# Optimization experiments

Hardware: AMD Instinct MI355X
Metric: run time of the kernel (lower is better)

The kernel has to match this reference:

```python
import jax, jax.numpy as jnp
import numpy as np
from math import sqrt

N = 8192      # points
I = 16        # in_channels
H = 64        # hidden_units
O = 64        # out_channels
CUTS = 8      # conv MLP intermediate width
RADIUS = 9.0
GROUPS = 4    # GroupNorm groups
BLK = 128     # i-block size for tiled pairwise reduction (KeOps-style)


def _leaky(x):
    return jnp.where(x >= 0, x, 0.2 * x)


def _group_norm(f, w, b, eps=1e-5):
    # torch GroupNorm applied to (1, C, N): stats per group over (C//G channels x N points)
    n, c = f.shape
    g = f.reshape(n, GROUPS, c // GROUPS)
    m = g.mean(axis=(0, 2), keepdims=True)
    v = ((g - m) ** 2).mean(axis=(0, 2), keepdims=True)
    g = (g - m) * jax.lax.rsqrt(v + eps)
    return g.reshape(n, c) * w + b


def setup_inputs() -> dict:
    key = jax.random.key(0)
    ks = jax.random.split(key, 20)
    U = lambda k, s, lim: jax.random.uniform(k, s, minval=-lim, maxval=lim)
    points = jax.random.normal(ks[0], (N, 3), dtype=jnp.float32)
    nuv = jax.random.normal(ks[1], (N, 3, 3), dtype=jnp.float32)
    features = jax.random.normal(ks[2], (N, I), dtype=jnp.float32)
    # net_in (torch Linear default init)
    W_in1 = U(ks[3], (H, I), 1 / np.sqrt(I)); b_in1 = U(ks[4], (H,), 1 / np.sqrt(I))
    W_in2 = U(ks[5], (H, H), 1 / np.sqrt(H)); b_in2 = U(ks[6], (H,), 1 / np.sqrt(H))
    # conv MLP with custom init from the module
    A1 = jax.random.normal(ks[7], (CUTS, 3), dtype=jnp.float32)
    B1 = jax.random.uniform(ks[8], (CUTS,)) * 0.8 * jnp.sqrt((A1 ** 2).sum(-1))
    A2 = U(ks[9], (H, CUTS), 1 / np.sqrt(CUTS))
    B2 = jax.random.normal(ks[10], (H,)) * 0.5 * jnp.sqrt((A2 ** 2).sum(-1))
    # net_out
    W_out1 = U(ks[11], (O, H), 1 / np.sqrt(H)); b_out1 = U(ks[12], (O,), 1 / np.sqrt(H))
    W_out2 = U(ks[13], (O, O), 1 / np.sqrt(O)); b_out2 = U(ks[14], (O,), 1 / np.sqrt(O))
    return {
        "points": points, "nuv": nuv, "features": features,
        "W_in1": W_in1, "b_in1": b_in1, "W_in2": W_in2, "b_in2": b_in2,
        "gn_in_w": jnp.ones((H,), jnp.float32), "gn_in_b": jnp.zeros((H,), jnp.float32),
        "A1": A1, "B1": B1, "A2": A2, "B2": B2,
        "W_out1": W_out1, "b_out1": b_out1, "W_out2": W_out2, "b_out2": b_out2,
        "gn_out_w": jnp.ones((O,), jnp.float32), "gn_out_b": jnp.zeros((O,), jnp.float32),
    }


def _forward(points, nuv, features, W_in1, b_in1, W_in2, b_in2, gn_in_w, gn_in_b,
             A1, B1, A2, B2, W_out1, b_out1, W_out2, b_out2, gn_out_w, gn_out_b):
    # 1. net_in + GroupNorm
    f = _leaky(features @ W_in1.T + b_in1)
    f = _leaky(f @ W_in2.T + b_in2)
    f = _group_norm(f, gn_in_w, gn_in_b)          # (N, H)
    # 2. quasi-geodesic interaction, tiled over i-blocks (KeOps-style)
    pts = points / (sqrt(2.0) * RADIUS)
    normals = jax.lax.stop_gradient(nuv[:, 0, :])  # n_j is detached in the original
    nblk = N // BLK

    def body(carry, blk):
        xi, nuvi = blk                              # (B,3), (B,3,3)
        ni = nuvi[:, 0, :]                          # (B,3) n_i (not detached)
        diff = pts[None, :, :] - xi[:, None, :]     # (B,N,3) x_j - x_i
        dn = ni @ normals.T                         # (B,N) <n_i, n_j>
        d2 = (diff ** 2).sum(-1) * (2.0 - dn) ** 2  # pseudo-geodesic squared dist
        w = jnp.exp(-d2)                            # Gaussian window
        X = jnp.einsum('bij,bnj->bni', nuvi, diff)  # coords in local basis (B,N,3)
        h = jax.nn.relu(jnp.einsum('bnj,cj->bnc', X, A1) + B1)   # (B,N,CUTS)
        g = jax.nn.relu(jnp.einsum('bnc,hc->bnh', h, A2) + B2)   # (B,N,H)
        out = jnp.einsum('bn,bnh,nh->bh', w, g, f)  # sum_j w_ij * conv(P_ij) * f_j
        return carry, out

    _, outs = jax.lax.scan(
        body, None, (pts.reshape(nblk, BLK, 3), nuv.reshape(nblk, BLK, 3, 3)))
    f2 = outs.reshape(N, H)
    # 3. net_out + GroupNorm
    f2 = _leaky(f2 @ W_out1.T + b_out1)
    f2 = _leaky(f2 @ W_out2.T + b_out2)
    f2 = _group_norm(f2, gn_out_w, gn_out_b)       # (N, O)
    return f2


def reference(points, nuv, features, W_in1, b_in1, W_in2, b_in2, gn_in_w, gn_in_b,
              A1, B1, A2, B2, W_out1, b_out1, W_out2, b_out2, gn_out_w, gn_out_b):
    return _forward(points, nuv, features, W_in1, b_in1, W_in2, b_in2, gn_in_w, gn_in_b,
                    A1, B1, A2, B2, W_out1, b_out1, W_out2, b_out2, gn_out_w, gn_out_b)
```

## Files before the change

### kernel.cpp

```cpp
#include <hip/hip_runtime.h>
#include <hip/hip_bf16.h>
#include <stdint.h>


#define N_PTS   8192
#define CHUNK   64
#define NCHUNK  (N_PTS / CHUNK)
#define WPB     8
#define PSCALE  0.07856742013183861f
#define GN_CNT  (N_PTS * 16)
#define FS_STRIDE 68

#define OFF_POINTS 0
#define OFF_NUV    24576
#define OFF_FEAT   98304
#define OFF_WIN1   229376
#define OFF_BIN1   230400
#define OFF_WIN2   230464
#define OFF_BIN2   234560
#define OFF_GNIW   234624
#define OFF_GNIB   234688
#define OFF_A1     234752
#define OFF_B1     234776
#define OFF_A2     234784
#define OFF_B2     235296
#define OFF_WOUT1  235360
#define OFF_BOUT1  239456
#define OFF_WOUT2  239520
#define OFF_BOUT2  243616
#define OFF_GNOW   243680
#define OFF_GNOB   243744
#define CVT_TOTAL  243808
#define NSEG 19

typedef _Float16 half2_t __attribute__((ext_vector_type(2)));
typedef _Float16 f16x8   __attribute__((ext_vector_type(8)));
typedef float    f32x4   __attribute__((ext_vector_type(4)));

struct InPtrs { const void* p[NSEG]; };

__device__ __forceinline__ float rfl(float x) {
  return __int_as_float(__builtin_amdgcn_readfirstlane(__float_as_int(x)));
}
__device__ __forceinline__ float leaky(float x) { return x > 0.f ? x : 0.2f * x; }

#if __has_builtin(__builtin_amdgcn_cvt_pkrtz)
__device__ __forceinline__ half2_t pk16(float a, float b) {
  return __builtin_bit_cast(half2_t, __builtin_amdgcn_cvt_pkrtz(a, b));
}
#else
__device__ __forceinline__ half2_t pk16(float a, float b) {
  half2_t r; r.x = (_Float16)a; r.y = (_Float16)b; return r;
}
#endif

__global__ __launch_bounds__(256) void prep_kernel(InPtrs ptrs, float* dst,
                                                   float* gstats) {
  if (blockIdx.x == 0 && threadIdx.x < 16) gstats[threadIdx.x] = 0.f;
  const uint32_t w0 = ((const uint32_t*)ptrs.p[7])[0];
  const bool bf = (w0 != 0x3F800000u);
  const int CUM[NSEG + 1] = {0, 24576, 98304, 229376, 230400, 230464, 234560,
                             234624, 234688, 234752, 234776, 234784, 235296,
                             235360, 239456, 239520, 243616, 243680, 243744,
                             243808};
  for (int e = blockIdx.x * 256 + threadIdx.x; e < CVT_TOTAL;
       e += gridDim.x * 256) {
    int s = 0;
#pragma unroll
    for (int i = 1; i < NSEG; ++i) s += (e >= CUM[i]) ? 1 : 0;
    const int rem = e - CUM[s];
    float v = bf ? __bfloat162float(((const __hip_bfloat16*)ptrs.p[s])[rem])
                 : ((const float*)ptrs.p[s])[rem];
    if (s == 0) v *= PSCALE;
    dst[e] = v;
  }
}

__global__ __launch_bounds__(256) void mlp_in_kernel(
    const float* __restrict__ pool, float* __restrict__ fbuf) {
  __shared__ float ls[4][64];
  const int t = threadIdx.x, nl = t >> 6, h = t & 63;
  const int n = blockIdx.x * 4 + nl;
  const float4* fr = (const float4*)(pool + OFF_FEAT + n * 16);
  const float4* w1 = (const float4*)(pool + OFF_WIN1 + h * 16);
  float a = pool[OFF_BIN1 + h];
#pragma unroll
  for (int k = 0; k < 4; ++k) {
    const float4 x = fr[k], w = w1[k];
    a = fmaf(x.x, w.x, a); a = fmaf(x.y, w.y, a);
    a = fmaf(x.z, w.z, a); a = fmaf(x.w, w.w, a);
  }
  ls[nl][h] = leaky(a);
  __syncthreads();
  const float4* w2 = (const float4*)(pool + OFF_WIN2 + h * 64);
  const float4* lr = (const float4*)&ls[nl][0];
  float c = pool[OFF_BIN2 + h];
#pragma unroll
  for (int k = 0; k < 16; ++k) {
    const float4 x = lr[k], w = w2[k];
    c = fmaf(x.x, w.x, c); c = fmaf(x.y, w.y, c);
    c = fmaf(x.z, w.z, c); c = fmaf(x.w, w.w, c);
  }
  fbuf[n * 64 + h] = leaky(c);
}

__global__ __launch_bounds__(256) void mlp_out_kernel(
    const float* __restrict__ cbuf, const float* __restrict__ pool,
    float* __restrict__ obuf) {
  __shared__ float ls[4][64];
  const int t = threadIdx.x, nl = t >> 6, h = t & 63;
  const int n = blockIdx.x * 4 + nl;
  const float4* cr = (const float4*)(cbuf + n * 64);
  const float4* w1 = (const float4*)(pool + OFF_WOUT1 + h * 64);
  float a = pool[OFF_BOUT1 + h];
#pragma unroll
  for (int k = 0; k < 16; ++k) {
    const float4 x = cr[k], w = w1[k];
    a = fmaf(x.x, w.x, a); a = fmaf(x.y, w.y, a);
    a = fmaf(x.z, w.z, a); a = fmaf(x.w, w.w, a);
  }
  ls[nl][h] = leaky(a);
  __syncthreads();
  const float4* w2 = (const float4*)(pool + OFF_WOUT2 + h * 64);
  const float4* lr = (const float4*)&ls[nl][0];
  float c = pool[OFF_BOUT2 + h];
#pragma unroll
  for (int k = 0; k < 16; ++k) {
    const float4 x = lr[k], w = w2[k];
    c = fmaf(x.x, w.x, c); c = fmaf(x.y, w.y, c);
    c = fmaf(x.z, w.z, c); c = fmaf(x.w, w.w, c);
  }
  obuf[n * 64 + h] = leaky(c);
}

__global__ __launch_bounds__(256) void gn_stats_kernel(
    const float* __restrict__ buf, float* __restrict__ gstats) {
  __shared__ float red[8];
  const int t = threadIdx.x;
  const int g = (t & 63) >> 4;
  if (t < 8) red[t] = 0.f;
  float s = 0.f, q = 0.f;
  for (int idx = blockIdx.x * 256 + t; idx < N_PTS * 64; idx += 64 * 256) {
    const float v = buf[idx];
    s += v; q = fmaf(v, v, q);
  }
  __syncthreads();
  atomicAdd(&red[g], s);
  atomicAdd(&red[4 + g], q);
  __syncthreads();
  if (t < 8) atomicAdd(&gstats[t], red[t]);
}

__global__ __launch_bounds__(256) void gn_apply_kernel(
    float* __restrict__ buf, const float* __restrict__ gstats,
    const float* __restrict__ pool) {
  const int idx = blockIdx.x * 256 + threadIdx.x;
  const int h = idx & 63, g = h >> 4;
  const float m = gstats[g] * (1.f / GN_CNT);
  const float v = gstats[4 + g] * (1.f / GN_CNT) - m * m;
  const float rs = rsqrtf(fmaxf(v, 0.f) + 1e-5f);
  buf[idx] = fmaf((buf[idx] - m) * rs, pool[OFF_GNIW + h], pool[OFF_GNIB + h]);
}

__global__ __launch_bounds__(256) void gn_apply_out_kernel(
    const float* __restrict__ buf, const float* __restrict__ gstats,
    const float* __restrict__ pool, void* __restrict__ out,
    const uint32_t* __restrict__ dref) {
  const bool bf = (dref[0] != 0x3F800000u);
  const int idx = blockIdx.x * 256 + threadIdx.x;
  const int h = idx & 63, g = h >> 4;
  const float m = gstats[g] * (1.f / GN_CNT);
  const float v = gstats[4 + g] * (1.f / GN_CNT) - m * m;
  const float rs = rsqrtf(fmaxf(v, 0.f) + 1e-5f);
  const float r = fmaf((buf[idx] - m) * rs, pool[OFF_GNOW + h], pool[OFF_GNOB + h]);
  if (bf) ((__hip_bfloat16*)out)[idx] = __float2bfloat16(r);
  else    ((float*)out)[idx] = r;
}

__global__ __launch_bounds__(512) void conv_kernel(
    const float* __restrict__ pool, const float* __restrict__ fbuf,
    float* __restrict__ cbuf) {
  __shared__ float  f_s[CHUNK * FS_STRIDE];
  __shared__ float4 hcA[WPB][4][32];
  __shared__ float4 zero4_s;

  const int t = threadIdx.x;
  const int wv = t >> 6, lane = t & 63;
  const int b = blockIdx.x * WPB + wv;
  const int kg  = lane >> 4;
  const int l15 = lane & 15;

  const float pbx = rfl(pool[OFF_POINTS + b * 3 + 0]);
  const float pby = rfl(pool[OFF_POINTS + b * 3 + 1]);
  const float pbz = rfl(pool[OFF_POINTS + b * 3 + 2]);
  float nb[9];
#pragma unroll
  for (int i = 0; i < 9; ++i) nb[i] = rfl(pool[OFF_NUV + b * 9 + i]);
  float a1v[24], b1v[8];
#pragma unroll
  for (int i = 0; i < 24; ++i) a1v[i] = rfl(pool[OFF_A1 + i]);
#pragma unroll
  for (int i = 0; i < 8; ++i)  b1v[i] = rfl(pool[OFF_B1 + i]);

  f16x8 bfrag[4];
#pragma unroll
  for (int ht = 0; ht < 4; ++ht) {
    const int h = 16 * ht + l15;
#pragma unroll
    for (int i = 0; i < 8; ++i) {
      float v = 0.f;
      if (kg == 0) v = pool[OFF_A2 + h * 8 + i];
      else if (kg == 1 && i == 0) v = pool[OFF_B2 + h];
      bfrag[ht][i] = (_Float16)v;
    }
  }

  {
    float4 z4; z4.x = 0.f; z4.y = 0.f; z4.z = 0.f; z4.w = 0.f;
    if (lane < 32) {
#pragma unroll
      for (int jt = 0; jt < 4; ++jt) hcA[wv][jt][lane] = z4;
    }
    if (t == 0) zero4_s = z4;
  }

  const f32x4 kzero = {0.f, 0.f, 0.f, 0.f};
  float acc[4] = {0.f, 0.f, 0.f, 0.f};
  const float4* fg4 = (const float4*)fbuf;

  for (int c = 0; c < NCHUNK; ++c) {
    const float4 fv0 = fg4[c * 1024 + t];
    const float4 fv1 = fg4[c * 1024 + t + 512];
    const int n = c * CHUNK + lane;
    const float px = pool[OFF_POINTS + n * 3 + 0];
    const float py = pool[OFF_POINTS + n * 3 + 1];
    const float pz = pool[OFF_POINTS + n * 3 + 2];
    const float nx = pool[OFF_NUV + n * 9 + 0];
    const float ny = pool[OFF_NUV + n * 9 + 1];
    const float nz = pool[OFF_NUV + n * 9 + 2];

    __syncthreads();
    ((float4*)f_s)[(t >> 4) * 17 + (t & 15)]        = fv0;
    ((float4*)f_s)[((t >> 4) + 32) * 17 + (t & 15)] = fv1;

    const float dx = px - pbx, dy = py - pby, dz = pz - pbz;
    const float X0 = fmaf(nb[0], dx, fmaf(nb[1], dy, nb[2] * dz));
    const float X1 = fmaf(nb[3], dx, fmaf(nb[4], dy, nb[5] * dz));
    const float X2 = fmaf(nb[6], dx, fmaf(nb[7], dy, nb[8] * dz));
    const float dn = fmaf(nb[0], nx, fmaf(nb[1], ny, nb[2] * nz));
    const float dd = fmaf(dx, dx, fmaf(dy, dy, dz * dz));
    const float tt = 2.f - dn;
    const float w = __expf(-dd * tt * tt);

    float hc[8];
#pragma unroll
    for (int cc = 0; cc < 8; ++cc)
      hc[cc] = w * fmaxf(fmaf(X0, a1v[cc * 3 + 0],
                         fmaf(X1, a1v[cc * 3 + 1],
                         fmaf(X2, a1v[cc * 3 + 2], b1v[cc]))), 0.f);
    float4 lo;
    lo.x = __builtin_bit_cast(float, pk16(hc[0], hc[1]));
    lo.y = __builtin_bit_cast(float, pk16(hc[2], hc[3]));
    lo.z = __builtin_bit_cast(float, pk16(hc[4], hc[5]));
    lo.w = __builtin_bit_cast(float, pk16(hc[6], hc[7]));
    hcA[wv][lane >> 4][l15] = lo;
    ((float*)&hcA[wv][lane >> 4][16 + l15])[0] =
        __builtin_bit_cast(float, pk16(w, 0.f));

    __syncthreads();

#pragma unroll
    for (int jt = 0; jt < 4; ++jt) {
      const float4* ap = (kg < 2) ? &hcA[wv][jt][kg * 16 + l15] : &zero4_s;
      const f16x8 af = __builtin_bit_cast(f16x8, *ap);
      const int fbase = (16 * jt + kg * 4) * FS_STRIDE + l15;
#pragma unroll
      for (int ht = 0; ht < 4; ++ht) {
        const f32x4 D = __builtin_amdgcn_mfma_f32_16x16x32_f16(
            af, bfrag[ht], kzero, 0, 0, 0);
        const float* fb = &f_s[fbase + 16 * ht];
#pragma unroll
        for (int r = 0; r < 4; ++r)
          acc[ht] = fmaf(fb[r * FS_STRIDE], fmaxf(D[r], 0.f), acc[ht]);
      }
    }
  }

#pragma unroll
  for (int ht = 0; ht < 4; ++ht) {
    acc[ht] += __shfl_xor(acc[ht], 16, 64);
    acc[ht] += __shfl_xor(acc[ht], 32, 64);
  }
  if (lane < 16) {
#pragma unroll
    for (int ht = 0; ht < 4; ++ht)
      cbuf[b * 64 + 16 * ht + lane] = acc[ht];
  }
}

extern "C" void kernel_launch(void* const* d_in, const int* in_sizes, int n_in,
                              void* d_out, int out_size, void* d_ws, size_t ws_size,
                              hipStream_t stream) {
  (void)in_sizes; (void)n_in; (void)out_size; (void)ws_size;
  const uint32_t* dref = (const uint32_t*)d_in[7];

  float* pool   = (float*)d_ws;
  float* fbuf   = pool + CVT_TOTAL;
  float* cbuf   = fbuf + N_PTS * 64;
  float* gstats = cbuf + N_PTS * 64;

  InPtrs ptrs;
  for (int i = 0; i < NSEG; ++i) ptrs.p[i] = d_in[i];

  prep_kernel<<<256, 256, 0, stream>>>(ptrs, pool, gstats);
  mlp_in_kernel<<<N_PTS / 4, 256, 0, stream>>>(pool, fbuf);
  gn_stats_kernel<<<64, 256, 0, stream>>>(fbuf, gstats);
  gn_apply_kernel<<<N_PTS * 64 / 256, 256, 0, stream>>>(fbuf, gstats, pool);
  conv_kernel<<<N_PTS / WPB, 512, 0, stream>>>(pool, fbuf, cbuf);
  mlp_out_kernel<<<N_PTS / 4, 256, 0, stream>>>(cbuf, pool, fbuf);
  gn_stats_kernel<<<64, 256, 0, stream>>>(fbuf, gstats + 8);
  gn_apply_out_kernel<<<N_PTS * 64 / 256, 256, 0, stream>>>(
      fbuf, gstats + 8, pool, d_out, dref);
}
```

Before: 695.9 us.

## Fold local-frame transform into A1, prefetch chunk data, use smaller MFMA

The conv kernel now precomputes per-row matrices M = A1·nuv_i and offsets, so each pair needs only one 3x3 affine step instead of a frame projection followed by the A1 layer. Squared distance is computed from packed points with precomputed norms, which a new pack kernel writes. The next chunk's features, points and normals are software-prefetched across the barriers, the K=32 f16 MFMA is replaced by a K=16 variant that wastes fewer zero lanes, and the accumulation uses packed FMA with an occupancy hint added to launch bounds. The risks are cancellation in the |p|^2-2p·q expansion and more register pressure from the prefetch.

```diff
diff --git a/kernel.cpp b/kernel.cpp
--- a/kernel.cpp
+++ b/kernel.cpp
@@ -34,7 +34,8 @@
 #define NSEG 19
 
 typedef _Float16 half2_t __attribute__((ext_vector_type(2)));
-typedef _Float16 f16x8   __attribute__((ext_vector_type(8)));
+typedef _Float16 f16x4   __attribute__((ext_vector_type(4)));
+typedef float    f32x2   __attribute__((ext_vector_type(2)));
 typedef float    f32x4   __attribute__((ext_vector_type(4)));
 
 struct InPtrs { const void* p[NSEG]; };
@@ -74,6 +75,24 @@
     if (s == 0) v *= PSCALE;
     dst[e] = v;
   }
+}
+
+__global__ __launch_bounds__(256) void pack_kernel(
+    const float* __restrict__ pool, float4* __restrict__ ppk,
+    float4* __restrict__ npk) {
+  const int n = blockIdx.x * 256 + threadIdx.x;
+  const float px = pool[OFF_POINTS + n * 3 + 0];
+  const float py = pool[OFF_POINTS + n * 3 + 1];
+  const float pz = pool[OFF_POINTS + n * 3 + 2];
+  float4 p; p.x = px; p.y = py; p.z = pz;
+  p.w = fmaf(px, px, fmaf(py, py, pz * pz));
+  ppk[n] = p;
+  float4 q;
+  q.x = pool[OFF_NUV + n * 9 + 0];
+  q.y = pool[OFF_NUV + n * 9 + 1];
+  q.z = pool[OFF_NUV + n * 9 + 2];
+  q.w = 0.f;
+  npk[n] = q;
 }
 
 __global__ __launch_bounds__(256) void mlp_in_kernel(
@@ -177,12 +196,14 @@
   else    ((float*)out)[idx] = r;
 }
 
-__global__ __launch_bounds__(512) void conv_kernel(
+__global__ __launch_bounds__(512, 8) void conv_kernel(
     const float* __restrict__ pool, const float* __restrict__ fbuf,
-    float* __restrict__ cbuf) {
+    float* __restrict__ cbuf, const float4* __restrict__ ppk,
+    const float4* __restrict__ npk) {
   __shared__ float  f_s[CHUNK * FS_STRIDE];
-  __shared__ float4 hcA[WPB][4][32];
-  __shared__ float4 zero4_s;
+  __shared__ float4 hcA2[WPB][CHUNK];
+  __shared__ f32x2  hcW2[WPB][CHUNK];
+  __shared__ f32x2  zero2_s;
 
   const int t = threadIdx.x;
   const int wv = t >> 6, lane = t & 63;
@@ -196,105 +217,131 @@
   float nb[9];
 #pragma unroll
   for (int i = 0; i < 9; ++i) nb[i] = rfl(pool[OFF_NUV + b * 9 + i]);
-  float a1v[24], b1v[8];
-#pragma unroll
-  for (int i = 0; i < 24; ++i) a1v[i] = rfl(pool[OFF_A1 + i]);
-#pragma unroll
-  for (int i = 0; i < 8; ++i)  b1v[i] = rfl(pool[OFF_B1 + i]);
-
-  f16x8 bfrag[4];
+  const float pbsq = rfl(fmaf(pbx, pbx, fmaf(pby, pby, pbz * pbz)));
+
+  float mM[24], mc[8];
+#pragma unroll
+  for (int cc = 0; cc < 8; ++cc) {
+    const float a0 = pool[OFF_A1 + cc * 3 + 0];
+    const float a1 = pool[OFF_A1 + cc * 3 + 1];
+    const float a2 = pool[OFF_A1 + cc * 3 + 2];
+#pragma unroll
+    for (int j = 0; j < 3; ++j)
+      mM[cc * 3 + j] =
+          rfl(fmaf(a0, nb[j], fmaf(a1, nb[3 + j], a2 * nb[6 + j])));
+    mc[cc] = rfl(fmaf(-mM[cc * 3 + 0], pbx,
+                 fmaf(-mM[cc * 3 + 1], pby,
+                 fmaf(-mM[cc * 3 + 2], pbz, pool[OFF_B1 + cc]))));
+  }
+
+  f16x4 bfrag[4];
 #pragma unroll
   for (int ht = 0; ht < 4; ++ht) {
     const int h = 16 * ht + l15;
 #pragma unroll
-    for (int i = 0; i < 8; ++i) {
+    for (int i = 0; i < 4; ++i) {
+      const int k = 4 * kg + i;
       float v = 0.f;
-      if (kg == 0) v = pool[OFF_A2 + h * 8 + i];
-      else if (kg == 1 && i == 0) v = pool[OFF_B2 + h];
+      if (k < 8) v = pool[OFF_A2 + h * 8 + k];
+      else if (k == 8) v = pool[OFF_B2 + h];
       bfrag[ht][i] = (_Float16)v;
     }
   }
 
-  {
-    float4 z4; z4.x = 0.f; z4.y = 0.f; z4.z = 0.f; z4.w = 0.f;
-    if (lane < 32) {
-#pragma unroll
-      for (int jt = 0; jt < 4; ++jt) hcA[wv][jt][lane] = z4;
-    }
-    if (t == 0) zero4_s = z4;
-  }
-
+  if (t == 0) { zero2_s.x = 0.f; zero2_s.y = 0.f; }
+
+  f32x2 acc01[4], acc23[4];
+#pragma unroll
+  for (int ht = 0; ht < 4; ++ht) {
+    acc01[ht].x = 0.f; acc01[ht].y = 0.f;
+    acc23[ht].x = 0.f; acc23[ht].y = 0.f;
+  }
   const f32x4 kzero = {0.f, 0.f, 0.f, 0.f};
-  float acc[4] = {0.f, 0.f, 0.f, 0.f};
   const float4* fg4 = (const float4*)fbuf;
 
+  float4 fv0 = fg4[t];
+  float4 fv1 = fg4[t + 512];
+  float4 pv  = ppk[lane];
+  float4 nv  = npk[lane];
+
   for (int c = 0; c < NCHUNK; ++c) {
-    const float4 fv0 = fg4[c * 1024 + t];
-    const float4 fv1 = fg4[c * 1024 + t + 512];
-    const int n = c * CHUNK + lane;
-    const float px = pool[OFF_POINTS + n * 3 + 0];
-    const float py = pool[OFF_POINTS + n * 3 + 1];
-    const float pz = pool[OFF_POINTS + n * 3 + 2];
-    const float nx = pool[OFF_NUV + n * 9 + 0];
-    const float ny = pool[OFF_NUV + n * 9 + 1];
-    const float nz = pool[OFF_NUV + n * 9 + 2];
-
-    __syncthreads();
+    asm volatile("" ::: "memory");
+    __builtin_amdgcn_s_barrier();
+    asm volatile("" ::: "memory");
+
     ((float4*)f_s)[(t >> 4) * 17 + (t & 15)]        = fv0;
     ((float4*)f_s)[((t >> 4) + 32) * 17 + (t & 15)] = fv1;
 
-    const float dx = px - pbx, dy = py - pby, dz = pz - pbz;
-    const float X0 = fmaf(nb[0], dx, fmaf(nb[1], dy, nb[2] * dz));
-    const float X1 = fmaf(nb[3], dx, fmaf(nb[4], dy, nb[5] * dz));
-    const float X2 = fmaf(nb[6], dx, fmaf(nb[7], dy, nb[8] * dz));
-    const float dn = fmaf(nb[0], nx, fmaf(nb[1], ny, nb[2] * nz));
-    const float dd = fmaf(dx, dx, fmaf(dy, dy, dz * dz));
-    const float tt = 2.f - dn;
-    const float w = __expf(-dd * tt * tt);
-
+    const float dotp = fmaf(pv.x, pbx, fmaf(pv.y, pby, pv.z * pbz));
+    const float dd   = fmaf(-2.f, dotp, pv.w + pbsq);
+    const float dn   = fmaf(nb[0], nv.x, fmaf(nb[1], nv.y, nb[2] * nv.z));
+    const float ttv  = 2.f - dn;
+    const float wexp = __expf(-dd * ttv * ttv);
     float hc[8];
 #pragma unroll
     for (int cc = 0; cc < 8; ++cc)
-      hc[cc] = w * fmaxf(fmaf(X0, a1v[cc * 3 + 0],
-                         fmaf(X1, a1v[cc * 3 + 1],
-                         fmaf(X2, a1v[cc * 3 + 2], b1v[cc]))), 0.f);
-    float4 lo;
-    lo.x = __builtin_bit_cast(float, pk16(hc[0], hc[1]));
-    lo.y = __builtin_bit_cast(float, pk16(hc[2], hc[3]));
-    lo.z = __builtin_bit_cast(float, pk16(hc[4], hc[5]));
-    lo.w = __builtin_bit_cast(float, pk16(hc[6], hc[7]));
-    hcA[wv][lane >> 4][l15] = lo;
-    ((float*)&hcA[wv][lane >> 4][16 + l15])[0] =
-        __builtin_bit_cast(float, pk16(w, 0.f));
-
-    __syncthreads();
+      hc[cc] = wexp * fmaxf(fmaf(mM[cc * 3 + 0], pv.x,
+                            fmaf(mM[cc * 3 + 1], pv.y,
+                            fmaf(mM[cc * 3 + 2], pv.z, mc[cc]))), 0.f);
+    float4 av;
+    av.x = __builtin_bit_cast(float, pk16(hc[0], hc[1]));
+    av.y = __builtin_bit_cast(float, pk16(hc[2], hc[3]));
+    av.z = __builtin_bit_cast(float, pk16(hc[4], hc[5]));
+    av.w = __builtin_bit_cast(float, pk16(hc[6], hc[7]));
+    hcA2[wv][lane] = av;
+    f32x2 wv2;
+    wv2.x = __builtin_bit_cast(float, pk16(wexp, 0.f));
+    wv2.y = 0.f;
+    hcW2[wv][lane] = wv2;
+
+    const int cn = (c < NCHUNK - 1) ? c + 1 : c;
+    fv0 = fg4[cn * 1024 + t];
+    fv1 = fg4[cn * 1024 + t + 512];
+    pv  = ppk[cn * CHUNK + lane];
+    nv  = npk[cn * CHUNK + lane];
+
+    asm volatile("s_waitcnt lgkmcnt(0)" ::: "memory");
+    __builtin_amdgcn_s_barrier();
+    asm volatile("" ::: "memory");
 
 #pragma unroll
     for (int jt = 0; jt < 4; ++jt) {
-      const float4* ap = (kg < 2) ? &hcA[wv][jt][kg * 16 + l15] : &zero4_s;
-      const f16x8 af = __builtin_bit_cast(f16x8, *ap);
+      const f32x2* ap;
+      if (kg < 2)       ap = ((const f32x2*)&hcA2[wv][16 * jt + l15]) + kg;
+      else if (kg == 2) ap = &hcW2[wv][16 * jt + l15];
+      else              ap = &zero2_s;
+      const f16x4 af = __builtin_bit_cast(f16x4, *ap);
       const int fbase = (16 * jt + kg * 4) * FS_STRIDE + l15;
 #pragma unroll
       for (int ht = 0; ht < 4; ++ht) {
-        const f32x4 D = __builtin_amdgcn_mfma_f32_16x16x32_f16(
+        const f32x4 D = __builtin_amdgcn_mfma_f32_16x16x16f16(
             af, bfrag[ht], kzero, 0, 0, 0);
         const float* fb = &f_s[fbase + 16 * ht];
-#pragma unroll
-        for (int r = 0; r < 4; ++r)
-          acc[ht] = fmaf(fb[r * FS_STRIDE], fmaxf(D[r], 0.f), acc[ht]);
+        f32x2 fq01, fq23, q01, q23;
+        fq01.x = fb[0];             fq01.y = fb[FS_STRIDE];
+        fq23.x = fb[2 * FS_STRIDE]; fq23.y = fb[3 * FS_STRIDE];
+        q01.x = fmaxf(D[0], 0.f);   q01.y = fmaxf(D[1], 0.f);
+        q23.x = fmaxf(D[2], 0.f);   q23.y = fmaxf(D[3], 0.f);
+        asm("v_pk_fma_f32 %0, %1, %2, %0"
+            : "+v"(acc01[ht]) : "v"(fq01), "v"(q01));
+        asm("v_pk_fma_f32 %0, %1, %2, %0"
+            : "+v"(acc23[ht]) : "v"(fq23), "v"(q23));
       }
     }
   }
 
+  float accf[4];
 #pragma unroll
   for (int ht = 0; ht < 4; ++ht) {
-    acc[ht] += __shfl_xor(acc[ht], 16, 64);
-    acc[ht] += __shfl_xor(acc[ht], 32, 64);
+    float a = (acc01[ht].x + acc01[ht].y) + (acc23[ht].x + acc23[ht].y);
+    a += __shfl_xor(a, 16, 64);
+    a += __shfl_xor(a, 32, 64);
+    accf[ht] = a;
   }
   if (lane < 16) {
 #pragma unroll
     for (int ht = 0; ht < 4; ++ht)
-      cbuf[b * 64 + 16 * ht + lane] = acc[ht];
+      cbuf[b * 64 + 16 * ht + lane] = accf[ht];
   }
 }
 
@@ -308,15 +355,20 @@
   float* fbuf   = pool + CVT_TOTAL;
   float* cbuf   = fbuf + N_PTS * 64;
   float* gstats = cbuf + N_PTS * 64;
+  float* ppk    = gstats + 16;
+  float* npk    = ppk + N_PTS * 4;
 
   InPtrs ptrs;
   for (int i = 0; i < NSEG; ++i) ptrs.p[i] = d_in[i];
 
   prep_kernel<<<256, 256, 0, stream>>>(ptrs, pool, gstats);
+  pack_kernel<<<N_PTS / 256, 256, 0, stream>>>(pool, (float4*)ppk, (float4*)npk);
   mlp_in_kernel<<<N_PTS / 4, 256, 0, stream>>>(pool, fbuf);
   gn_stats_kernel<<<64, 256, 0, stream>>>(fbuf, gstats);
   gn_apply_kernel<<<N_PTS * 64 / 256, 256, 0, stream>>>(fbuf, gstats, pool);
-  conv_kernel<<<N_PTS / WPB, 512, 0, stream>>>(pool, fbuf, cbuf);
+  conv_kernel<<<N_PTS / WPB, 512, 0, stream>>>(pool, fbuf, cbuf,
+                                               (const float4*)ppk,
+                                               (const float4*)npk);
   mlp_out_kernel<<<N_PTS / 4, 256, 0, stream>>>(cbuf, pool, fbuf);
   gn_stats_kernel<<<64, 256, 0, stream>>>(fbuf, gstats + 8);
   gn_apply_out_kernel<<<N_PTS * 64 / 256, 256, 0, stream>>>(
```

Result: slower. 805.1 us (+15.7%).

## Transpose normalized features so conv kernel reads them with float4 LDS loads

Applied to the files above, without the earlier changes.

The GroupNorm apply kernel now writes the normalized features transposed (channel-major) into a new buffer through a shared-memory tile. The conv kernel stages these transposed chunks into LDS, so each MFMA output group can fetch its four feature values with a single float4 read instead of four strided scalar reads. This targets LDS instruction count in the hot inner loop. The cost is an extra transpose pass and a second feature buffer in the workspace, which assumes the workspace is large enough.

```diff
diff --git a/kernel.cpp b/kernel.cpp
--- a/kernel.cpp
+++ b/kernel.cpp
@@ -151,15 +151,43 @@
   if (t < 8) atomicAdd(&gstats[t], red[t]);
 }
 
-__global__ __launch_bounds__(256) void gn_apply_kernel(
-    float* __restrict__ buf, const float* __restrict__ gstats,
-    const float* __restrict__ pool) {
-  const int idx = blockIdx.x * 256 + threadIdx.x;
-  const int h = idx & 63, g = h >> 4;
+__global__ __launch_bounds__(256) void gn_apply_T_kernel(
+    const float* __restrict__ buf, const float* __restrict__ gstats,
+    const float* __restrict__ pool, float* __restrict__ bufT) {
+  __shared__ float tile[64][68];
+  const int t = threadIdx.x;
+  const int n0 = blockIdx.x * 64;
+  const int rr = t >> 4;
+  const int cc = (t & 15) * 4;
+  const int g = cc >> 4;
   const float m = gstats[g] * (1.f / GN_CNT);
   const float v = gstats[4 + g] * (1.f / GN_CNT) - m * m;
   const float rs = rsqrtf(fmaxf(v, 0.f) + 1e-5f);
-  buf[idx] = fmaf((buf[idx] - m) * rs, pool[OFF_GNIW + h], pool[OFF_GNIB + h]);
+  const float4 gw = *(const float4*)&pool[OFF_GNIW + cc];
+  const float4 gb = *(const float4*)&pool[OFF_GNIB + cc];
+#pragma unroll
+  for (int r = 0; r < 4; ++r) {
+    const int row = rr + 16 * r;
+    const float4 x = *(const float4*)&buf[(n0 + row) * 64 + cc];
+    float4 o;
+    o.x = fmaf((x.x - m) * rs, gw.x, gb.x);
+    o.y = fmaf((x.y - m) * rs, gw.y, gb.y);
+    o.z = fmaf((x.z - m) * rs, gw.z, gb.z);
+    o.w = fmaf((x.w - m) * rs, gw.w, gb.w);
+    *(float4*)&tile[row][cc] = o;
+  }
+  __syncthreads();
+  const int nb = (t & 15) * 4;
+#pragma unroll
+  for (int r = 0; r < 4; ++r) {
+    const int h = rr + 16 * r;
+    float4 o;
+    o.x = tile[nb + 0][h];
+    o.y = tile[nb + 1][h];
+    o.z = tile[nb + 2][h];
+    o.w = tile[nb + 3][h];
+    *(float4*)&bufT[h * N_PTS + n0 + nb] = o;
+  }
 }
 
 __global__ __launch_bounds__(256) void gn_apply_out_kernel(
@@ -178,9 +206,9 @@
 }
 
 __global__ __launch_bounds__(512) void conv_kernel(
-    const float* __restrict__ pool, const float* __restrict__ fbuf,
+    const float* __restrict__ pool, const float* __restrict__ fbufT,
     float* __restrict__ cbuf) {
-  __shared__ float  f_s[CHUNK * FS_STRIDE];
+  __shared__ float  f_t[CHUNK * FS_STRIDE];
   __shared__ float4 hcA[WPB][4][32];
   __shared__ float4 zero4_s;
 
@@ -226,11 +254,13 @@
 
   const f32x4 kzero = {0.f, 0.f, 0.f, 0.f};
   float acc[4] = {0.f, 0.f, 0.f, 0.f};
-  const float4* fg4 = (const float4*)fbuf;
+  const float4* ftg = (const float4*)fbufT;
+  const int srow = t >> 3;
+  const int scol = (t & 7) * 2;
 
   for (int c = 0; c < NCHUNK; ++c) {
-    const float4 fv0 = fg4[c * 1024 + t];
-    const float4 fv1 = fg4[c * 1024 + t + 512];
+    const float4 fv0 = ftg[srow * (N_PTS / 4) + c * 16 + scol];
+    const float4 fv1 = ftg[srow * (N_PTS / 4) + c * 16 + scol + 1];
     const int n = c * CHUNK + lane;
     const float px = pool[OFF_POINTS + n * 3 + 0];
     const float py = pool[OFF_POINTS + n * 3 + 1];
@@ -240,8 +270,8 @@
     const float nz = pool[OFF_NUV + n * 9 + 2];
 
     __syncthreads();
-    ((float4*)f_s)[(t >> 4) * 17 + (t & 15)]        = fv0;
-    ((float4*)f_s)[((t >> 4) + 32) * 17 + (t & 15)] = fv1;
+    ((float4*)f_t)[srow * 17 + scol]     = fv0;
+    ((float4*)f_t)[srow * 17 + scol + 1] = fv1;
 
     const float dx = px - pbx, dy = py - pby, dz = pz - pbz;
     const float X0 = fmaf(nb[0], dx, fmaf(nb[1], dy, nb[2] * dz));
@@ -273,15 +303,17 @@
     for (int jt = 0; jt < 4; ++jt) {
       const float4* ap = (kg < 2) ? &hcA[wv][jt][kg * 16 + l15] : &zero4_s;
       const f16x8 af = __builtin_bit_cast(f16x8, *ap);
-      const int fbase = (16 * jt + kg * 4) * FS_STRIDE + l15;
+      const int cbase = 16 * jt + 4 * kg;
 #pragma unroll
       for (int ht = 0; ht < 4; ++ht) {
         const f32x4 D = __builtin_amdgcn_mfma_f32_16x16x32_f16(
             af, bfrag[ht], kzero, 0, 0, 0);
-        const float* fb = &f_s[fbase + 16 * ht];
-#pragma unroll
-        for (int r = 0; r < 4; ++r)
-          acc[ht] = fmaf(fb[r * FS_STRIDE], fmaxf(D[r], 0.f), acc[ht]);
+        const float4 fv =
+            *(const float4*)&f_t[(16 * ht + l15) * FS_STRIDE + cbase];
+        acc[ht] = fmaf(fv.x, fmaxf(D[0], 0.f), acc[ht]);
+        acc[ht] = fmaf(fv.y, fmaxf(D[1], 0.f), acc[ht]);
+        acc[ht] = fmaf(fv.z, fmaxf(D[2], 0.f), acc[ht]);
+        acc[ht] = fmaf(fv.w, fmaxf(D[3], 0.f), acc[ht]);
       }
     }
   }
@@ -308,6 +340,7 @@
   float* fbuf   = pool + CVT_TOTAL;
   float* cbuf   = fbuf + N_PTS * 64;
   float* gstats = cbuf + N_PTS * 64;
+  float* fbufT  = gstats + 16;
 
   InPtrs ptrs;
   for (int i = 0; i < NSEG; ++i) ptrs.p[i] = d_in[i];
@@ -315,8 +348,8 @@
   prep_kernel<<<256, 256, 0, stream>>>(ptrs, pool, gstats);
   mlp_in_kernel<<<N_PTS / 4, 256, 0, stream>>>(pool, fbuf);
   gn_stats_kernel<<<64, 256, 0, stream>>>(fbuf, gstats);
-  gn_apply_kernel<<<N_PTS * 64 / 256, 256, 0, stream>>>(fbuf, gstats, pool);
-  conv_kernel<<<N_PTS / WPB, 512, 0, stream>>>(pool, fbuf, cbuf);
+  gn_apply_T_kernel<<<N_PTS / 64, 256, 0, stream>>>(fbuf, gstats, pool, fbufT);
+  conv_kernel<<<N_PTS / WPB, 512, 0, stream>>>(pool, fbufT, cbuf);
   mlp_out_kernel<<<N_PTS / 4, 256, 0, stream>>>(cbuf, pool, fbuf);
   gn_stats_kernel<<<64, 256, 0, stream>>>(fbuf, gstats + 8);
   gn_apply_out_kernel<<<N_PTS * 64 / 256, 256, 0, stream>>>(
```

Result: slower. 756.6 us (+8.7%).
